# Optimization experiments

Measured on AMD Instinct MI355X. Metric: run time of the kernel, lower is better.

Reference implementation:

```python
import jax, jax.numpy as jnp
import numpy as np

NEG_BIG = 1e20


def setup_inputs() -> dict:
    key = jax.random.key(0)
    k1, k2, k3 = jax.random.split(key, 3)
    B, Tenc, Tdec, D = 8, 2048, 512, 1024
    enc = jax.random.normal(k1, (B, Tenc, D), dtype=jnp.float32)
    dec = jax.random.normal(k2, (B, Tdec, D), dtype=jnp.float32)
    enc_mask = jax.random.randint(k3, (B, Tenc), 0, 2, dtype=jnp.int32)
    # guarantee at least one valid position per row to keep softmax well-defined
    enc_mask = enc_mask.at[:, 0].set(1)
    return {"enc": enc, "enc_mask": enc_mask, "dec": dec}


def reference(enc, enc_mask, dec):
    # dropout=0 and identity transforms -> enc_trans = enc, dec_trans = dec
    mask = enc_mask.astype(enc.dtype)  # (B, Tenc)
    # raw scores: sum_d dec[b,u,d] * enc[b,t,d] -> (B, Tenc, Tdec)
    raw = jnp.einsum('btd,bud->btu', enc, dec)
    raw = raw - (1.0 - mask)[:, :, None] * NEG_BIG
    scores = jax.nn.softmax(raw, axis=1)  # softmax over Tenc
    # context: sum_t scores[b,t,u] * enc[b,t,d] -> (B, Tdec, D)
    context = jnp.einsum('btu,btd->bud', scores, enc)
    return context, scores
```

## Files before the change

kernel.cpp:

```cpp
#include <hip/hip_runtime.h>
#include <math.h>

#define BATCH 8
#define TENC 2048
#define TDEC 512
#define DIM 1024
#define NEG_BIG 1e20f

typedef __attribute__((ext_vector_type(8))) short short8;
typedef __attribute__((ext_vector_type(4))) float f32x4;
typedef unsigned short ushort_t;

__device__ __forceinline__ unsigned int bf16rn(float x) {
    unsigned int u = __float_as_uint(x);
    return (u + 0x7FFFu + ((u >> 16) & 1u)) >> 16;
}
__device__ __forceinline__ float bf16f(unsigned int b) {
    return __uint_as_float(b << 16);
}
__device__ __forceinline__ void split2(float x, unsigned int& h, unsigned int& l) {
    h = bf16rn(x);
    l = bf16rn(x - bf16f(h));
}

#define GLOAD16(g, l)                                                        \
    __builtin_amdgcn_global_load_lds(                                        \
        (const __attribute__((address_space(1))) unsigned int*)(g),          \
        (__attribute__((address_space(3))) unsigned int*)(l), 16, 0, 0)

__device__ __forceinline__ size_t tiled_off(int row, int k, int ntK) {
    return ((size_t)(row >> 4) * ntK + (k >> 5)) * 512
         + ((k >> 3) & 3) * 128 + (row & 15) * 8;
}


__global__ __launch_bounds__(256) void prep_fused(
    const float* __restrict__ enc, const float* __restrict__ dec,
    ushort_t* __restrict__ encH, ushort_t* __restrict__ encL,
    ushort_t* __restrict__ encT, ushort_t* __restrict__ decH,
    ushort_t* __restrict__ decL)
{
    __shared__ ushort_t T[64][72];

    const int b   = blockIdx.z;
    const int d0  = blockIdx.x * 64;
    const int tid = threadIdx.x;

    if (blockIdx.y < 32) {
        const int t0 = blockIdx.y * 64;
        const float* E = enc + (size_t)b * TENC * DIM;
        const size_t bofs1 = (size_t)b * TENC * DIM;
        const size_t bofs2 = (size_t)b * DIM * TENC;

        const int ltr = tid >> 2;
#pragma unroll
        for (int it = 0; it < 2; ++it) {
            const int c  = (tid & 3) + it * 4;
            const int gt = t0 + ltr;
            const int gd = d0 + c * 8;
            float4 x0 = *(const float4*)&E[(size_t)gt * DIM + gd];
            float4 x1 = *(const float4*)&E[(size_t)gt * DIM + gd + 4];
            float xs[8] = {x0.x, x0.y, x0.z, x0.w, x1.x, x1.y, x1.z, x1.w};
            unsigned int h[8], l[8];
            short8 hv, lv;
#pragma unroll
            for (int j = 0; j < 8; ++j) {
                split2(xs[j], h[j], l[j]);
                hv[j] = (short)h[j];
                lv[j] = (short)l[j];
            }
            const size_t off = bofs1 + tiled_off(gt, gd, DIM / 32);
            *(short8*)&encH[off] = hv;
            *(short8*)&encL[off] = lv;
#pragma unroll
            for (int j = 0; j < 8; ++j) T[c * 8 + j][ltr] = (ushort_t)h[j];
        }
        __syncthreads();

        const int dr = tid >> 2;
#pragma unroll
        for (int it = 0; it < 2; ++it) {
            const int tc = (tid & 3) + it * 4;
            const int gd = d0 + dr;
            const int gt = t0 + tc * 8;
            short8 v = *(const short8*)&T[dr][tc * 8];
            *(short8*)&encT[bofs2 + tiled_off(gd, gt, TENC / 32)] = v;
        }
    } else {
        const int u0 = (blockIdx.y - 32) * 64;
        const float* D = dec + (size_t)b * TDEC * DIM;
        const size_t bofs = (size_t)b * TDEC * DIM;

        const int lur = tid >> 2;
#pragma unroll
        for (int it = 0; it < 2; ++it) {
            const int c  = (tid & 3) + it * 4;
            const int gu = u0 + lur;
            const int gd = d0 + c * 8;
            float4 x0 = *(const float4*)&D[(size_t)gu * DIM + gd];
            float4 x1 = *(const float4*)&D[(size_t)gu * DIM + gd + 4];
            float xs[8] = {x0.x, x0.y, x0.z, x0.w, x1.x, x1.y, x1.z, x1.w};
            short8 hv, lv;
#pragma unroll
            for (int j = 0; j < 8; ++j) {
                unsigned int h, l;
                split2(xs[j], h, l);
                hv[j] = (short)h;
                lv[j] = (short)l;
            }
            const size_t off = bofs + tiled_off(gu, gd, DIM / 32);
            *(short8*)&decH[off] = hv;
            *(short8*)&decL[off] = lv;
        }
    }
}

__global__ __launch_bounds__(256) void gemm1_lds(
    const ushort_t* __restrict__ encH, const ushort_t* __restrict__ encL,
    const ushort_t* __restrict__ decH, const ushort_t* __restrict__ decL,
    const int* __restrict__ mask, float* __restrict__ raw,
    float* __restrict__ pm, float* __restrict__ ps)
{
    __shared__ __align__(16) ushort_t Ah[128 * 32];
    __shared__ __align__(16) ushort_t Al[128 * 32];
    __shared__ __align__(16) ushort_t Bh[128 * 32];
    __shared__ __align__(16) ushort_t Bl[128 * 32];
    __shared__ float smx[4][68];
    __shared__ float ssx[4][68];

    const int b  = blockIdx.x;
    const int m0 = blockIdx.y * 128;
    const int n0 = blockIdx.z * 128;
    const int tid = threadIdx.x;

    const int lane = tid & 63;
    const int w    = tid >> 6;
    const int wm   = (w & 1) * 64;
    const int wn   = (w >> 1) * 64;
    const int lr   = lane & 15;
    const int q    = lane >> 4;
    const int l8   = lane * 8;

    const int fa = wm * 32 + q * 128 + lr * 8;
    const int fb = wn * 32 + q * 128 + lr * 8;

    const ushort_t* AH = encH + (size_t)b * TENC * DIM;
    const ushort_t* AL = encL + (size_t)b * TENC * DIM;
    const ushort_t* BH = decH + (size_t)b * TDEC * DIM;
    const ushort_t* BL = decL + (size_t)b * TDEC * DIM;
    float* C = raw + (size_t)b * TENC * TDEC;

    f32x4 acc[4][4] = {};

    for (int k0 = 0; k0 < DIM; k0 += 32) {
        __syncthreads();
#pragma unroll
        for (int q2 = 0; q2 < 2; ++q2) {
            const int rg = w * 2 + q2;
            const size_t tA = ((size_t)((m0 >> 4) + rg) * (DIM / 32) + (k0 >> 5)) * 512 + l8;
            const size_t tB = ((size_t)((n0 >> 4) + rg) * (DIM / 32) + (k0 >> 5)) * 512 + l8;
            GLOAD16(AH + tA, &Ah[rg * 512]);
            GLOAD16(AL + tA, &Al[rg * 512]);
            GLOAD16(BH + tB, &Bh[rg * 512]);
            GLOAD16(BL + tB, &Bl[rg * 512]);
        }
        __syncthreads();

        short8 ah[4], al[4], bh[4], bl[4];
#pragma unroll
        for (int i = 0; i < 4; ++i) {
            ah[i] = *(const short8*)&Ah[fa + i * 512];
            al[i] = *(const short8*)&Al[fa + i * 512];
            bh[i] = *(const short8*)&Bh[fb + i * 512];
            bl[i] = *(const short8*)&Bl[fb + i * 512];
        }
#pragma unroll
        for (int i = 0; i < 4; ++i)
#pragma unroll
            for (int j = 0; j < 4; ++j) {
                acc[i][j] = __builtin_amdgcn_mfma_f32_16x16x32_bf16(ah[i], bh[j], acc[i][j], 0, 0, 0);
                acc[i][j] = __builtin_amdgcn_mfma_f32_16x16x32_bf16(ah[i], bl[j], acc[i][j], 0, 0, 0);
                acc[i][j] = __builtin_amdgcn_mfma_f32_16x16x32_bf16(al[i], bh[j], acc[i][j], 0, 0, 0);
            }
    }

    float mkv[4][4];
#pragma unroll
    for (int i = 0; i < 4; ++i)
#pragma unroll
        for (int rr = 0; rr < 4; ++rr) {
            const int t = m0 + wm + i * 16 + q * 4 + rr;
            mkv[i][rr] = (mask[b * TENC + t] == 0) ? NEG_BIG : 0.0f;
        }

    float cm[4] = {-INFINITY, -INFINITY, -INFINITY, -INFINITY};
    float cs[4] = {0.f, 0.f, 0.f, 0.f};
#pragma unroll
    for (int i = 0; i < 4; ++i)
#pragma unroll
        for (int rr = 0; rr < 4; ++rr) {
            const int t = m0 + wm + i * 16 + q * 4 + rr;
#pragma unroll
            for (int j = 0; j < 4; ++j) {
                const int u = n0 + wn + j * 16 + lr;
                const float v = acc[i][j][rr] - mkv[i][rr];
                C[(size_t)t * TDEC + u] = v;
                cm[j] = fmaxf(cm[j], v);
            }
        }
#pragma unroll
    for (int i = 0; i < 4; ++i)
#pragma unroll
        for (int rr = 0; rr < 4; ++rr)
#pragma unroll
            for (int j = 0; j < 4; ++j)
                cs[j] += __expf(acc[i][j][rr] - mkv[i][rr] - cm[j]);

#pragma unroll
    for (int j = 0; j < 4; ++j) {
#pragma unroll
        for (int d = 16; d < 64; d <<= 1) {
            float om = __shfl_xor(cm[j], d, 64);
            float os = __shfl_xor(cs[j], d, 64);
            float mn = fmaxf(cm[j], om);
            cs[j] = cs[j] * __expf(cm[j] - mn) + os * __expf(om - mn);
            cm[j] = mn;
        }
    }

    if (q == 0) {
#pragma unroll
        for (int j = 0; j < 4; ++j) {
            smx[w][j * 16 + lr] = cm[j];
            ssx[w][j * 16 + lr] = cs[j];
        }
    }
    __syncthreads();
    if (tid < 128) {
        const int col = tid;
        const int wp  = (col >> 6) * 2;
        const int ci  = col & 63;
        const float m1 = smx[wp][ci],     s1 = ssx[wp][ci];
        const float m2 = smx[wp + 1][ci], s2 = ssx[wp + 1][ci];
        const float M = fmaxf(m1, m2);
        const float S = s1 * __expf(m1 - M) + s2 * __expf(m2 - M);
        const int idx = b * TDEC + n0 + col;
        const int tb  = m0 >> 7;
        pm[(size_t)tb * (BATCH * TDEC) + idx] = M;
        ps[(size_t)tb * (BATCH * TDEC) + idx] = S;
    }
}

__global__ __launch_bounds__(256) void norm_kernel(
    float* __restrict__ S, const float* __restrict__ pm,
    const float* __restrict__ ps, ushort_t* __restrict__ scoresT)
{
    __shared__ ushort_t T[64][72];
    __shared__ float cMs[64], cIs[64];

    const int b  = blockIdx.z;
    const int t0 = blockIdx.x * 64;
    const int u0 = blockIdx.y * 64;
    const int tid = threadIdx.x;

    if (tid < 64) {
        const int idx = b * TDEC + u0 + tid;
        float M = -INFINITY;
#pragma unroll
        for (int z = 0; z < 16; ++z)
            M = fmaxf(M, pm[(size_t)z * (BATCH * TDEC) + idx]);
        float s = 0.0f;
#pragma unroll
        for (int z = 0; z < 16; ++z)
            s += ps[(size_t)z * (BATCH * TDEC) + idx] *
                 __expf(pm[(size_t)z * (BATCH * TDEC) + idx] - M);
        cMs[tid] = M;
        cIs[tid] = 1.0f / s;
    }
    __syncthreads();

    const int tr  = tid >> 4;
    const int ucl = (tid & 15) * 4;

    float4 M4 = *(const float4*)&cMs[ucl];
    float4 I4 = *(const float4*)&cIs[ucl];

    float* base = S + (size_t)b * TENC * TDEC;

#pragma unroll
    for (int i = 0; i < 4; ++i) {
        const int t = t0 + tr + 16 * i;
        float4 x = *(const float4*)&base[(size_t)t * TDEC + u0 + ucl];
        float4 p;
        p.x = __expf(x.x - M4.x) * I4.x;
        p.y = __expf(x.y - M4.y) * I4.y;
        p.z = __expf(x.z - M4.z) * I4.z;
        p.w = __expf(x.w - M4.w) * I4.w;
        *(float4*)&base[(size_t)t * TDEC + u0 + ucl] = p;
        const int tloc = tr + 16 * i;
        T[ucl + 0][tloc] = (ushort_t)bf16rn(p.x);
        T[ucl + 1][tloc] = (ushort_t)bf16rn(p.y);
        T[ucl + 2][tloc] = (ushort_t)bf16rn(p.z);
        T[ucl + 3][tloc] = (ushort_t)bf16rn(p.w);
    }
    __syncthreads();

    const size_t bofs = (size_t)b * TDEC * TENC;
    const int ur = tid >> 2;
#pragma unroll
    for (int it = 0; it < 2; ++it) {
        const int tc = (tid & 3) + it * 4;
        const int gu = u0 + ur;
        const int gt = t0 + tc * 8;
        short8 v = *(const short8*)&T[ur][tc * 8];
        *(short8*)&scoresT[bofs + tiled_off(gu, gt, TENC / 32)] = v;
    }
}

__global__ __launch_bounds__(256) void gemm2_lds(
    const ushort_t* __restrict__ scoresT, const ushort_t* __restrict__ encT,
    ushort_t* __restrict__ p0, ushort_t* __restrict__ p1,
    ushort_t* __restrict__ p2, ushort_t* __restrict__ p3)
{
    __shared__ __align__(16) ushort_t Ah[128 * 32];
    __shared__ __align__(16) ushort_t Bh[128 * 32];

    const int b  = blockIdx.x;
    const int ks = blockIdx.y >> 3;
    const int n0 = (blockIdx.y & 7) * 128;
    const int m0 = blockIdx.z * 128;
    const int tid = threadIdx.x;

    const int lane = tid & 63;
    const int w    = tid >> 6;
    const int wm   = (w & 1) * 64;
    const int wn   = (w >> 1) * 64;
    const int lr   = lane & 15;
    const int q    = lane >> 4;
    const int l8   = lane * 8;

    const int fa = wm * 32 + q * 128 + lr * 8;
    const int fb = wn * 32 + q * 128 + lr * 8;

    const ushort_t* A = scoresT + (size_t)b * TDEC * TENC;
    const ushort_t* B = encT    + (size_t)b * DIM * TENC;
    ushort_t* Psel = ks == 0 ? p0 : (ks == 1 ? p1 : (ks == 2 ? p2 : p3));
    ushort_t* P = Psel + (size_t)b * TDEC * DIM;

    const int kbeg = ks * (TENC / 4);
    const int kend = kbeg + TENC / 4;

    f32x4 acc[4][4] = {};

    for (int k0 = kbeg; k0 < kend; k0 += 32) {
        __syncthreads();
#pragma unroll
        for (int q2 = 0; q2 < 2; ++q2) {
            const int rg = w * 2 + q2;
            const size_t tA = ((size_t)((m0 >> 4) + rg) * (TENC / 32) + (k0 >> 5)) * 512 + l8;
            const size_t tB = ((size_t)((n0 >> 4) + rg) * (TENC / 32) + (k0 >> 5)) * 512 + l8;
            GLOAD16(A + tA, &Ah[rg * 512]);
            GLOAD16(B + tB, &Bh[rg * 512]);
        }
        __syncthreads();

        short8 ah[4], bh[4];
#pragma unroll
        for (int i = 0; i < 4; ++i) {
            ah[i] = *(const short8*)&Ah[fa + i * 512];
            bh[i] = *(const short8*)&Bh[fb + i * 512];
        }
#pragma unroll
        for (int i = 0; i < 4; ++i)
#pragma unroll
            for (int j = 0; j < 4; ++j)
                acc[i][j] = __builtin_amdgcn_mfma_f32_16x16x32_bf16(ah[i], bh[j], acc[i][j], 0, 0, 0);
    }

#pragma unroll
    for (int i = 0; i < 4; ++i)
#pragma unroll
        for (int rr = 0; rr < 4; ++rr) {
            const int u = m0 + wm + i * 16 + q * 4 + rr;
#pragma unroll
            for (int j = 0; j < 4; ++j) {
                const int d = n0 + wn + j * 16 + lr;
                P[(size_t)u * DIM + d] = (ushort_t)bf16rn(acc[i][j][rr]);
            }
        }
}

__global__ __launch_bounds__(256) void reduce_ctx(
    const ushort_t* __restrict__ p0, const ushort_t* __restrict__ p1,
    const ushort_t* __restrict__ p2, const ushort_t* __restrict__ p3,
    float* __restrict__ ctx)
{
    const size_t i8 = ((size_t)blockIdx.x * 256 + threadIdx.x) * 8;
    short8 a = *(const short8*)(p0 + i8);
    short8 b = *(const short8*)(p1 + i8);
    short8 c = *(const short8*)(p2 + i8);
    short8 d = *(const short8*)(p3 + i8);
    float o[8];
#pragma unroll
    for (int j = 0; j < 8; ++j)
        o[j] = bf16f((unsigned short)a[j]) + bf16f((unsigned short)b[j])
             + bf16f((unsigned short)c[j]) + bf16f((unsigned short)d[j]);
    *(float4*)(ctx + i8)     = make_float4(o[0], o[1], o[2], o[3]);
    *(float4*)(ctx + i8 + 4) = make_float4(o[4], o[5], o[6], o[7]);
}


__device__ __forceinline__ void store8(ushort_t* ph, ushort_t* pl,
                                       float4 x0, float4 x1) {
    float xs[8] = {x0.x, x0.y, x0.z, x0.w, x1.x, x1.y, x1.z, x1.w};
    short8 hv, lv;
#pragma unroll
    for (int i = 0; i < 8; ++i) {
        unsigned int h, l;
        split2(xs[i], h, l);
        hv[i] = (short)h;
        lv[i] = (short)l;
    }
    *(short8*)ph = hv;
    *(short8*)pl = lv;
}

__device__ __forceinline__ void wr4(ushort_t* ph, ushort_t* pl, const float* x) {
    unsigned int h[4], l[4];
#pragma unroll
    for (int i = 0; i < 4; ++i) split2(x[i], h[i], l[i]);
    *(uint2*)ph = make_uint2(h[0] | (h[1] << 16), h[2] | (h[3] << 16));
    *(uint2*)pl = make_uint2(l[0] | (l[1] << 16), l[2] | (l[3] << 16));
}

__device__ __forceinline__ short8 frag8B(const ushort_t* p) {
    union { short8 v; uint2 u[2]; } f;
    f.u[0] = *(const uint2*)p;
    f.u[1] = *(const uint2*)(p + 4);
    return f.v;
}

__global__ __launch_bounds__(256) void gemm1_mfma(
    const float* __restrict__ enc, const float* __restrict__ dec,
    const int* __restrict__ mask, float* __restrict__ raw)
{
    __shared__ __align__(16) ushort_t Ah[128 * 32];
    __shared__ __align__(16) ushort_t Al[128 * 32];
    __shared__ __align__(16) ushort_t Bh[128 * 32];
    __shared__ __align__(16) ushort_t Bl[128 * 32];

    const int b  = blockIdx.z;
    const int m0 = blockIdx.y * 128;
    const int n0 = blockIdx.x * 128;
    const int tid = threadIdx.x;

    const float* A  = enc + (size_t)b * TENC * DIM;
    const float* Bg = dec + (size_t)b * TDEC * DIM;
    float*       C  = raw + (size_t)b * TENC * TDEC;

    const int lane = tid & 63;
    const int wv   = tid >> 6;
    const int wm   = (wv & 1) * 64;
    const int wn   = (wv >> 1) * 64;
    const int lr   = lane & 15;
    const int q    = lane >> 4;

    const int r0 = tid >> 2;
    const int c8 = (tid & 3) * 8;

    f32x4 acc[4][4] = {};

    for (int k0 = 0; k0 < DIM; k0 += 32) {
        const float* pa0 = A  + (size_t)(m0 + r0) * DIM + k0 + c8;
        const float* pa1 = A  + (size_t)(m0 + r0 + 64) * DIM + k0 + c8;
        const float* pb0 = Bg + (size_t)(n0 + r0) * DIM + k0 + c8;
        const float* pb1 = Bg + (size_t)(n0 + r0 + 64) * DIM + k0 + c8;
        float4 a0 = *(const float4*)pa0, a0b = *(const float4*)(pa0 + 4);
        float4 a1 = *(const float4*)pa1, a1b = *(const float4*)(pa1 + 4);
        float4 b0 = *(const float4*)pb0, b0b = *(const float4*)(pb0 + 4);
        float4 b1 = *(const float4*)pb1, b1b = *(const float4*)(pb1 + 4);

        __syncthreads();
        store8(&Ah[r0 * 32 + c8],        &Al[r0 * 32 + c8],        a0, a0b);
        store8(&Ah[(r0 + 64) * 32 + c8], &Al[(r0 + 64) * 32 + c8], a1, a1b);
        store8(&Bh[r0 * 32 + c8],        &Bl[r0 * 32 + c8],        b0, b0b);
        store8(&Bh[(r0 + 64) * 32 + c8], &Bl[(r0 + 64) * 32 + c8], b1, b1b);
        __syncthreads();

        short8 ah[4], al[4], bh[4], bl[4];
#pragma unroll
        for (int i = 0; i < 4; ++i) {
            ah[i] = *(const short8*)&Ah[(wm + i * 16 + lr) * 32 + q * 8];
            al[i] = *(const short8*)&Al[(wm + i * 16 + lr) * 32 + q * 8];
            bh[i] = *(const short8*)&Bh[(wn + i * 16 + lr) * 32 + q * 8];
            bl[i] = *(const short8*)&Bl[(wn + i * 16 + lr) * 32 + q * 8];
        }
#pragma unroll
        for (int i = 0; i < 4; ++i)
#pragma unroll
            for (int j = 0; j < 4; ++j) {
                acc[i][j] = __builtin_amdgcn_mfma_f32_16x16x32_bf16(ah[i], bh[j], acc[i][j], 0, 0, 0);
                acc[i][j] = __builtin_amdgcn_mfma_f32_16x16x32_bf16(ah[i], bl[j], acc[i][j], 0, 0, 0);
                acc[i][j] = __builtin_amdgcn_mfma_f32_16x16x32_bf16(al[i], bh[j], acc[i][j], 0, 0, 0);
            }
    }

#pragma unroll
    for (int i = 0; i < 4; ++i)
#pragma unroll
        for (int rr = 0; rr < 4; ++rr) {
            const int t = m0 + wm + i * 16 + q * 4 + rr;
            const float mk = (mask[b * TENC + t] == 0) ? NEG_BIG : 0.0f;
#pragma unroll
            for (int j = 0; j < 4; ++j) {
                const int u = n0 + wn + j * 16 + lr;
                C[(size_t)t * TDEC + u] = acc[i][j][rr] - mk;
            }
        }
}

__global__ __launch_bounds__(256) void softmax_kernel(float* __restrict__ S)
{
    const int b  = blockIdx.y;
    const int u0 = blockIdx.x * 16;
    const int up = threadIdx.x & 15;
    const int tg = threadIdx.x >> 4;

    float* col = S + (size_t)b * TENC * TDEC + u0;

    float m = -INFINITY, s = 0.0f;
    for (int t = tg; t < TENC; t += 16) {
        float x = col[(size_t)t * TDEC + up];
        float mn = fmaxf(m, x);
        s = s * __expf(m - mn) + __expf(x - mn);
        m = mn;
    }

    __shared__ float sm[16][17];
    __shared__ float ss[16][17];
    sm[tg][up] = m;
    ss[tg][up] = s;
    __syncthreads();

    float M = -INFINITY;
#pragma unroll
    for (int j = 0; j < 16; ++j) M = fmaxf(M, sm[j][up]);
    float sum = 0.0f;
#pragma unroll
    for (int j = 0; j < 16; ++j) sum += ss[j][up] * __expf(sm[j][up] - M);
    const float inv = 1.0f / sum;

    for (int t = tg; t < TENC; t += 16) {
        float x = col[(size_t)t * TDEC + up];
        col[(size_t)t * TDEC + up] = __expf(x - M) * inv;
    }
}

#define G2_LD 36

__global__ __launch_bounds__(256) void gemm2_mfma(
    const float* __restrict__ scores, const float* __restrict__ enc,
    float* __restrict__ context)
{
    __shared__ __align__(16) ushort_t Ah[128 * G2_LD];
    __shared__ __align__(16) ushort_t Al[128 * G2_LD];
    __shared__ __align__(16) ushort_t Bh[128 * G2_LD];
    __shared__ __align__(16) ushort_t Bl[128 * G2_LD];

    const int b  = blockIdx.z;
    const int m0 = blockIdx.y * 128;
    const int n0 = blockIdx.x * 128;
    const int tid = threadIdx.x;

    const float* S = scores + (size_t)b * TENC * TDEC;
    const float* E = enc    + (size_t)b * TENC * DIM;
    float*       C = context + (size_t)b * TDEC * DIM;

    const int lane = tid & 63;
    const int wv   = tid >> 6;
    const int wm   = (wv & 1) * 64;
    const int wn   = (wv >> 1) * 64;
    const int lr   = lane & 15;
    const int q    = lane >> 4;

    const int ul = tid & 127;
    const int th = (tid >> 7) * 16;

    f32x4 acc[4][4] = {};

    for (int k0 = 0; k0 < TENC; k0 += 32) {
        float av[16], bv[16];
#pragma unroll
        for (int i = 0; i < 4; ++i) {
            const int t = k0 + th + i * 4;
#pragma unroll
            for (int j = 0; j < 4; ++j) {
                av[i * 4 + j] = S[(size_t)(t + j) * TDEC + m0 + ul];
                bv[i * 4 + j] = E[(size_t)(t + j) * DIM + n0 + ul];
            }
        }
        __syncthreads();
#pragma unroll
        for (int i = 0; i < 4; ++i) {
            const int tt = th + i * 4;
            wr4(&Ah[ul * G2_LD + tt], &Al[ul * G2_LD + tt], &av[i * 4]);
            wr4(&Bh[ul * G2_LD + tt], &Bl[ul * G2_LD + tt], &bv[i * 4]);
        }
        __syncthreads();

        short8 ah[4], al[4], bh[4], bl[4];
#pragma unroll
        for (int i = 0; i < 4; ++i) {
            ah[i] = frag8B(&Ah[(wm + i * 16 + lr) * G2_LD + q * 8]);
            al[i] = frag8B(&Al[(wm + i * 16 + lr) * G2_LD + q * 8]);
            bh[i] = frag8B(&Bh[(wn + i * 16 + lr) * G2_LD + q * 8]);
            bl[i] = frag8B(&Bl[(wn + i * 16 + lr) * G2_LD + q * 8]);
        }
#pragma unroll
        for (int i = 0; i < 4; ++i)
#pragma unroll
            for (int j = 0; j < 4; ++j) {
                acc[i][j] = __builtin_amdgcn_mfma_f32_16x16x32_bf16(ah[i], bh[j], acc[i][j], 0, 0, 0);
                acc[i][j] = __builtin_amdgcn_mfma_f32_16x16x32_bf16(ah[i], bl[j], acc[i][j], 0, 0, 0);
                acc[i][j] = __builtin_amdgcn_mfma_f32_16x16x32_bf16(al[i], bh[j], acc[i][j], 0, 0, 0);
            }
    }

#pragma unroll
    for (int i = 0; i < 4; ++i)
#pragma unroll
        for (int rr = 0; rr < 4; ++rr) {
            const int u = m0 + wm + i * 16 + q * 4 + rr;
#pragma unroll
            for (int j = 0; j < 4; ++j) {
                const int d = n0 + wn + j * 16 + lr;
                C[(size_t)u * DIM + d] = acc[i][j][rr];
            }
        }
}

extern "C" void kernel_launch(void* const* d_in, const int* in_sizes, int n_in,
                              void* d_out, int out_size, void* d_ws, size_t ws_size,
                              hipStream_t stream)
{
    const float* enc      = (const float*)d_in[0];
    const int*   enc_mask = (const int*)  d_in[1];
    const float* dec      = (const float*)d_in[2];

    float* context = (float*)d_out;
    float* scores  = context + (size_t)BATCH * TDEC * DIM;

    const size_t OFF_ENC_H = 0;
    const size_t OFF_ENC_L = 33554432;
    const size_t OFF_DEC_H = 67108864;
    const size_t OFF_DEC_L = 75497472;
    const size_t OFF_ENC_T = 83886080;
    const size_t OFF_SCO_T = 117440512;
    const size_t WS_NEED   = 134217728;

    if (ws_size >= WS_NEED) {
        char* w = (char*)d_ws;
        ushort_t* encH    = (ushort_t*)(w + OFF_ENC_H);
        ushort_t* encL    = (ushort_t*)(w + OFF_ENC_L);
        ushort_t* decH    = (ushort_t*)(w + OFF_DEC_H);
        ushort_t* decL    = (ushort_t*)(w + OFF_DEC_L);
        ushort_t* encT    = (ushort_t*)(w + OFF_ENC_T);
        ushort_t* scoresT = (ushort_t*)(w + OFF_SCO_T);
        ushort_t* part0   = (ushort_t*)(w + OFF_ENC_H);
        ushort_t* part1   = (ushort_t*)(w + OFF_ENC_H + 8388608);
        ushort_t* part2   = (ushort_t*)(w + OFF_ENC_H + 16777216);
        ushort_t* part3   = (ushort_t*)(w + OFF_ENC_H + 25165824);
        float*    pm      = context;
        float*    ps      = context + 65536;

        prep_fused<<<dim3(DIM / 64, 40, BATCH), 256, 0, stream>>>(
            enc, dec, encH, encL, encT, decH, decL);

        gemm1_lds<<<dim3(BATCH, TENC / 128, TDEC / 128), 256, 0, stream>>>(
            encH, encL, decH, decL, enc_mask, scores, pm, ps);

        norm_kernel<<<dim3(TENC / 64, TDEC / 64, BATCH), 256, 0, stream>>>(
            scores, pm, ps, scoresT);

        gemm2_lds<<<dim3(BATCH, 32, TDEC / 128), 256, 0, stream>>>(
            scoresT, encT, part0, part1, part2, part3);

        reduce_ctx<<<2048, 256, 0, stream>>>(part0, part1, part2, part3, context);
    } else {
        gemm1_mfma<<<dim3(TDEC / 128, TENC / 128, BATCH), 256, 0, stream>>>(
            enc, dec, enc_mask, scores);
        softmax_kernel<<<dim3(TDEC / 16, BATCH), 256, 0, stream>>>(scores);
        gemm2_mfma<<<dim3(DIM / 128, TDEC / 128, BATCH), 256, 0, stream>>>(
            scores, enc, context);
    }
}
```

Measured before the change: 233.2 us.

## Switch to fp16 split operands, store exp'd fp16 probabilities, widen gemm2 tile

Replaces the three-pass bf16 hi/lo split with fp16, keeping only enc high and dec high+low, so gemm1 issues two MFMAs per tile instead of three and no longer loads encL. Gemm1 now computes the block max first, then writes exp(x-M) as fp16 probabilities instead of fp32 raw scores. The norm kernel then only rescales by a per-block weight, which halves that intermediate traffic and avoids recomputing exp. Gemm2 uses 256-wide N tiles with fewer blocks and fp16 MFMA. The risks are fp16 range and precision loss in the scores, since small exp values can underflow, and higher register pressure in gemm2.

```diff
diff --git a/kernel.cpp b/kernel.cpp
--- a/kernel.cpp
+++ b/kernel.cpp
@@ -11,6 +11,17 @@
 typedef __attribute__((ext_vector_type(4))) float f32x4;
 typedef unsigned short ushort_t;
 
+__device__ __forceinline__ ushort_t f16bits(float x) {
+    union { _Float16 h; ushort_t u; } cv;
+    cv.h = (_Float16)x;
+    return cv.u;
+}
+__device__ __forceinline__ float f16val(ushort_t u) {
+    union { _Float16 h; ushort_t u; } cv;
+    cv.u = u;
+    return (float)cv.h;
+}
+
 __device__ __forceinline__ unsigned int bf16rn(float x) {
     unsigned int u = __float_as_uint(x);
     return (u + 0x7FFFu + ((u >> 16) & 1u)) >> 16;
@@ -36,9 +47,8 @@
 
 __global__ __launch_bounds__(256) void prep_fused(
     const float* __restrict__ enc, const float* __restrict__ dec,
-    ushort_t* __restrict__ encH, ushort_t* __restrict__ encL,
-    ushort_t* __restrict__ encT, ushort_t* __restrict__ decH,
-    ushort_t* __restrict__ decL)
+    ushort_t* __restrict__ encH, ushort_t* __restrict__ encT,
+    ushort_t* __restrict__ decH, ushort_t* __restrict__ decL)
 {
     __shared__ ushort_t T[64][72];
 
@@ -61,19 +71,12 @@
             float4 x0 = *(const float4*)&E[(size_t)gt * DIM + gd];
             float4 x1 = *(const float4*)&E[(size_t)gt * DIM + gd + 4];
             float xs[8] = {x0.x, x0.y, x0.z, x0.w, x1.x, x1.y, x1.z, x1.w};
-            unsigned int h[8], l[8];
-            short8 hv, lv;
-#pragma unroll
-            for (int j = 0; j < 8; ++j) {
-                split2(xs[j], h[j], l[j]);
-                hv[j] = (short)h[j];
-                lv[j] = (short)l[j];
-            }
-            const size_t off = bofs1 + tiled_off(gt, gd, DIM / 32);
-            *(short8*)&encH[off] = hv;
-            *(short8*)&encL[off] = lv;
-#pragma unroll
-            for (int j = 0; j < 8; ++j) T[c * 8 + j][ltr] = (ushort_t)h[j];
+            short8 hv;
+#pragma unroll
+            for (int j = 0; j < 8; ++j) hv[j] = (short)f16bits(xs[j]);
+            *(short8*)&encH[bofs1 + tiled_off(gt, gd, DIM / 32)] = hv;
+#pragma unroll
+            for (int j = 0; j < 8; ++j) T[c * 8 + j][ltr] = (ushort_t)hv[j];
         }
         __syncthreads();
 
@@ -81,10 +84,8 @@
 #pragma unroll
         for (int it = 0; it < 2; ++it) {
             const int tc = (tid & 3) + it * 4;
-            const int gd = d0 + dr;
-            const int gt = t0 + tc * 8;
             short8 v = *(const short8*)&T[dr][tc * 8];
-            *(short8*)&encT[bofs2 + tiled_off(gd, gt, TENC / 32)] = v;
+            *(short8*)&encT[bofs2 + tiled_off(d0 + dr, t0 + tc * 8, TENC / 32)] = v;
         }
     } else {
         const int u0 = (blockIdx.y - 32) * 64;
@@ -103,10 +104,9 @@
             short8 hv, lv;
 #pragma unroll
             for (int j = 0; j < 8; ++j) {
-                unsigned int h, l;
-                split2(xs[j], h, l);
+                ushort_t h = f16bits(xs[j]);
                 hv[j] = (short)h;
-                lv[j] = (short)l;
+                lv[j] = (short)f16bits(xs[j] - f16val(h));
             }
             const size_t off = bofs + tiled_off(gu, gd, DIM / 32);
             *(short8*)&decH[off] = hv;
@@ -116,13 +116,11 @@
 }
 
 __global__ __launch_bounds__(256) void gemm1_lds(
-    const ushort_t* __restrict__ encH, const ushort_t* __restrict__ encL,
-    const ushort_t* __restrict__ decH, const ushort_t* __restrict__ decL,
-    const int* __restrict__ mask, float* __restrict__ raw,
-    float* __restrict__ pm, float* __restrict__ ps)
+    const ushort_t* __restrict__ encH, const ushort_t* __restrict__ decH,
+    const ushort_t* __restrict__ decL, const int* __restrict__ mask,
+    ushort_t* __restrict__ p16, float* __restrict__ pm, float* __restrict__ ps)
 {
     __shared__ __align__(16) ushort_t Ah[128 * 32];
-    __shared__ __align__(16) ushort_t Al[128 * 32];
     __shared__ __align__(16) ushort_t Bh[128 * 32];
     __shared__ __align__(16) ushort_t Bl[128 * 32];
     __shared__ float smx[4][68];
@@ -145,10 +143,9 @@
     const int fb = wn * 32 + q * 128 + lr * 8;
 
     const ushort_t* AH = encH + (size_t)b * TENC * DIM;
-    const ushort_t* AL = encL + (size_t)b * TENC * DIM;
     const ushort_t* BH = decH + (size_t)b * TDEC * DIM;
     const ushort_t* BL = decL + (size_t)b * TDEC * DIM;
-    float* C = raw + (size_t)b * TENC * TDEC;
+    ushort_t* P = p16 + (size_t)b * TENC * TDEC;
 
     f32x4 acc[4][4] = {};
 
@@ -160,17 +157,15 @@
             const size_t tA = ((size_t)((m0 >> 4) + rg) * (DIM / 32) + (k0 >> 5)) * 512 + l8;
             const size_t tB = ((size_t)((n0 >> 4) + rg) * (DIM / 32) + (k0 >> 5)) * 512 + l8;
             GLOAD16(AH + tA, &Ah[rg * 512]);
-            GLOAD16(AL + tA, &Al[rg * 512]);
             GLOAD16(BH + tB, &Bh[rg * 512]);
             GLOAD16(BL + tB, &Bl[rg * 512]);
         }
         __syncthreads();
 
-        short8 ah[4], al[4], bh[4], bl[4];
+        short8 ah[4], bh[4], bl[4];
 #pragma unroll
         for (int i = 0; i < 4; ++i) {
             ah[i] = *(const short8*)&Ah[fa + i * 512];
-            al[i] = *(const short8*)&Al[fa + i * 512];
             bh[i] = *(const short8*)&Bh[fb + i * 512];
             bl[i] = *(const short8*)&Bl[fb + i * 512];
         }
@@ -178,9 +173,8 @@
         for (int i = 0; i < 4; ++i)
 #pragma unroll
             for (int j = 0; j < 4; ++j) {
-                acc[i][j] = __builtin_amdgcn_mfma_f32_16x16x32_bf16(ah[i], bh[j], acc[i][j], 0, 0, 0);
-                acc[i][j] = __builtin_amdgcn_mfma_f32_16x16x32_bf16(ah[i], bl[j], acc[i][j], 0, 0, 0);
-                acc[i][j] = __builtin_amdgcn_mfma_f32_16x16x32_bf16(al[i], bh[j], acc[i][j], 0, 0, 0);
+                acc[i][j] = __builtin_amdgcn_mfma_f32_16x16x32_f16(ah[i], bh[j], acc[i][j], 0, 0, 0);
+                acc[i][j] = __builtin_amdgcn_mfma_f32_16x16x32_f16(ah[i], bl[j], acc[i][j], 0, 0, 0);
             }
     }
 
@@ -194,6 +188,28 @@
         }
 
     float cm[4] = {-INFINITY, -INFINITY, -INFINITY, -INFINITY};
+#pragma unroll
+    for (int i = 0; i < 4; ++i)
+#pragma unroll
+        for (int rr = 0; rr < 4; ++rr)
+#pragma unroll
+            for (int j = 0; j < 4; ++j)
+                cm[j] = fmaxf(cm[j], acc[i][j][rr] - mkv[i][rr]);
+#pragma unroll
+    for (int j = 0; j < 4; ++j) {
+        cm[j] = fmaxf(cm[j], __shfl_xor(cm[j], 16, 64));
+        cm[j] = fmaxf(cm[j], __shfl_xor(cm[j], 32, 64));
+    }
+    if (q == 0) {
+#pragma unroll
+        for (int j = 0; j < 4; ++j) smx[w][j * 16 + lr] = cm[j];
+    }
+    __syncthreads();
+    float M[4];
+#pragma unroll
+    for (int j = 0; j < 4; ++j)
+        M[j] = fmaxf(smx[w][j * 16 + lr], smx[w ^ 1][j * 16 + lr]);
+
     float cs[4] = {0.f, 0.f, 0.f, 0.f};
 #pragma unroll
     for (int i = 0; i < 4; ++i)
@@ -203,64 +219,46 @@
 #pragma unroll
             for (int j = 0; j < 4; ++j) {
                 const int u = n0 + wn + j * 16 + lr;
-                const float v = acc[i][j][rr] - mkv[i][rr];
-                C[(size_t)t * TDEC + u] = v;
-                cm[j] = fmaxf(cm[j], v);
-            }
-        }
-#pragma unroll
-    for (int i = 0; i < 4; ++i)
-#pragma unroll
-        for (int rr = 0; rr < 4; ++rr)
-#pragma unroll
-            for (int j = 0; j < 4; ++j)
-                cs[j] += __expf(acc[i][j][rr] - mkv[i][rr] - cm[j]);
-
+                const float p = __expf(acc[i][j][rr] - mkv[i][rr] - M[j]);
+                cs[j] += p;
+                P[(size_t)t * TDEC + u] = f16bits(p);
+            }
+        }
 #pragma unroll
     for (int j = 0; j < 4; ++j) {
-#pragma unroll
-        for (int d = 16; d < 64; d <<= 1) {
-            float om = __shfl_xor(cm[j], d, 64);
-            float os = __shfl_xor(cs[j], d, 64);
-            float mn = fmaxf(cm[j], om);
-            cs[j] = cs[j] * __expf(cm[j] - mn) + os * __expf(om - mn);
-            cm[j] = mn;
-        }
-    }
-
+        cs[j] += __shfl_xor(cs[j], 16, 64);
+        cs[j] += __shfl_xor(cs[j], 32, 64);
+    }
     if (q == 0) {
 #pragma unroll
-        for (int j = 0; j < 4; ++j) {
-            smx[w][j * 16 + lr] = cm[j];
-            ssx[w][j * 16 + lr] = cs[j];
-        }
+        for (int j = 0; j < 4; ++j) ssx[w][j * 16 + lr] = cs[j];
     }
     __syncthreads();
     if (tid < 128) {
         const int col = tid;
         const int wp  = (col >> 6) * 2;
         const int ci  = col & 63;
-        const float m1 = smx[wp][ci],     s1 = ssx[wp][ci];
-        const float m2 = smx[wp + 1][ci], s2 = ssx[wp + 1][ci];
-        const float M = fmaxf(m1, m2);
-        const float S = s1 * __expf(m1 - M) + s2 * __expf(m2 - M);
+        const float Mf = fmaxf(smx[wp][ci], smx[wp + 1][ci]);
+        const float Sf = ssx[wp][ci] + ssx[wp + 1][ci];
         const int idx = b * TDEC + n0 + col;
         const int tb  = m0 >> 7;
-        pm[(size_t)tb * (BATCH * TDEC) + idx] = M;
-        ps[(size_t)tb * (BATCH * TDEC) + idx] = S;
+        pm[(size_t)tb * (BATCH * TDEC) + idx] = Mf;
+        ps[(size_t)tb * (BATCH * TDEC) + idx] = Sf;
     }
 }
 
 __global__ __launch_bounds__(256) void norm_kernel(
-    float* __restrict__ S, const float* __restrict__ pm,
-    const float* __restrict__ ps, ushort_t* __restrict__ scoresT)
+    const ushort_t* __restrict__ p16, float* __restrict__ scores,
+    const float* __restrict__ pm, const float* __restrict__ ps,
+    ushort_t* __restrict__ scoresT)
 {
     __shared__ ushort_t T[64][72];
-    __shared__ float cMs[64], cIs[64];
+    __shared__ float cW[64];
 
     const int b  = blockIdx.z;
     const int t0 = blockIdx.x * 64;
     const int u0 = blockIdx.y * 64;
+    const int tb = t0 >> 7;
     const int tid = threadIdx.x;
 
     if (tid < 64) {
@@ -274,34 +272,34 @@
         for (int z = 0; z < 16; ++z)
             s += ps[(size_t)z * (BATCH * TDEC) + idx] *
                  __expf(pm[(size_t)z * (BATCH * TDEC) + idx] - M);
-        cMs[tid] = M;
-        cIs[tid] = 1.0f / s;
+        cW[tid] = __expf(pm[(size_t)tb * (BATCH * TDEC) + idx] - M) / s;
     }
     __syncthreads();
 
     const int tr  = tid >> 4;
     const int ucl = (tid & 15) * 4;
 
-    float4 M4 = *(const float4*)&cMs[ucl];
-    float4 I4 = *(const float4*)&cIs[ucl];
-
-    float* base = S + (size_t)b * TENC * TDEC;
+    const float w0 = cW[ucl + 0], w1 = cW[ucl + 1];
+    const float w2 = cW[ucl + 2], w3 = cW[ucl + 3];
+
+    const ushort_t* Pb = p16 + (size_t)b * TENC * TDEC;
+    float* Sb = scores + (size_t)b * TENC * TDEC;
 
 #pragma unroll
     for (int i = 0; i < 4; ++i) {
         const int t = t0 + tr + 16 * i;
-        float4 x = *(const float4*)&base[(size_t)t * TDEC + u0 + ucl];
-        float4 p;
-        p.x = __expf(x.x - M4.x) * I4.x;
-        p.y = __expf(x.y - M4.y) * I4.y;
-        p.z = __expf(x.z - M4.z) * I4.z;
-        p.w = __expf(x.w - M4.w) * I4.w;
-        *(float4*)&base[(size_t)t * TDEC + u0 + ucl] = p;
+        ushort4 pv = *(const ushort4*)&Pb[(size_t)t * TDEC + u0 + ucl];
+        float4 sc;
+        sc.x = f16val(pv.x) * w0;
+        sc.y = f16val(pv.y) * w1;
+        sc.z = f16val(pv.z) * w2;
+        sc.w = f16val(pv.w) * w3;
+        *(float4*)&Sb[(size_t)t * TDEC + u0 + ucl] = sc;
         const int tloc = tr + 16 * i;
-        T[ucl + 0][tloc] = (ushort_t)bf16rn(p.x);
-        T[ucl + 1][tloc] = (ushort_t)bf16rn(p.y);
-        T[ucl + 2][tloc] = (ushort_t)bf16rn(p.z);
-        T[ucl + 3][tloc] = (ushort_t)bf16rn(p.w);
+        T[ucl + 0][tloc] = f16bits(sc.x);
+        T[ucl + 1][tloc] = f16bits(sc.y);
+        T[ucl + 2][tloc] = f16bits(sc.z);
+        T[ucl + 3][tloc] = f16bits(sc.w);
     }
     __syncthreads();
 
@@ -310,10 +308,8 @@
 #pragma unroll
     for (int it = 0; it < 2; ++it) {
         const int tc = (tid & 3) + it * 4;
-        const int gu = u0 + ur;
-        const int gt = t0 + tc * 8;
         short8 v = *(const short8*)&T[ur][tc * 8];
-        *(short8*)&scoresT[bofs + tiled_off(gu, gt, TENC / 32)] = v;
+        *(short8*)&scoresT[bofs + tiled_off(u0 + ur, t0 + tc * 8, TENC / 32)] = v;
     }
 }
 
@@ -323,18 +319,18 @@
     ushort_t* __restrict__ p2, ushort_t* __restrict__ p3)
 {
     __shared__ __align__(16) ushort_t Ah[128 * 32];
-    __shared__ __align__(16) ushort_t Bh[128 * 32];
+    __shared__ __align__(16) ushort_t Bh[256 * 32];
 
     const int b  = blockIdx.x;
-    const int ks = blockIdx.y >> 3;
-    const int n0 = (blockIdx.y & 7) * 128;
+    const int ks = blockIdx.y >> 2;
+    const int n0 = (blockIdx.y & 3) * 256;
     const int m0 = blockIdx.z * 128;
     const int tid = threadIdx.x;
 
     const int lane = tid & 63;
     const int w    = tid >> 6;
     const int wm   = (w & 1) * 64;
-    const int wn   = (w >> 1) * 64;
+    const int wn   = (w >> 1) * 128;
     const int lr   = lane & 15;
     const int q    = lane >> 4;
     const int l8   = lane * 8;
@@ -350,7 +346,7 @@
     const int kbeg = ks * (TENC / 4);
     const int kend = kbeg + TENC / 4;
 
-    f32x4 acc[4][4] = {};
+    f32x4 acc[4][8] = {};
 
     for (int k0 = kbeg; k0 < kend; k0 += 32) {
         __syncthreads();
@@ -358,23 +354,26 @@
         for (int q2 = 0; q2 < 2; ++q2) {
             const int rg = w * 2 + q2;
             const size_t tA = ((size_t)((m0 >> 4) + rg) * (TENC / 32) + (k0 >> 5)) * 512 + l8;
+            GLOAD16(A + tA, &Ah[rg * 512]);
+        }
+#pragma unroll
+        for (int q2 = 0; q2 < 4; ++q2) {
+            const int rg = w * 4 + q2;
             const size_t tB = ((size_t)((n0 >> 4) + rg) * (TENC / 32) + (k0 >> 5)) * 512 + l8;
-            GLOAD16(A + tA, &Ah[rg * 512]);
             GLOAD16(B + tB, &Bh[rg * 512]);
         }
         __syncthreads();
 
-        short8 ah[4], bh[4];
-#pragma unroll
-        for (int i = 0; i < 4; ++i) {
-            ah[i] = *(const short8*)&Ah[fa + i * 512];
-            bh[i] = *(const short8*)&Bh[fb + i * 512];
-        }
+        short8 av[4], bv[8];
+#pragma unroll
+        for (int i = 0; i < 4; ++i) av[i] = *(const short8*)&Ah[fa + i * 512];
+#pragma unroll
+        for (int j = 0; j < 8; ++j) bv[j] = *(const short8*)&Bh[fb + j * 512];
 #pragma unroll
         for (int i = 0; i < 4; ++i)
 #pragma unroll
-            for (int j = 0; j < 4; ++j)
-                acc[i][j] = __builtin_amdgcn_mfma_f32_16x16x32_bf16(ah[i], bh[j], acc[i][j], 0, 0, 0);
+            for (int j = 0; j < 8; ++j)
+                acc[i][j] = __builtin_amdgcn_mfma_f32_16x16x32_f16(av[i], bv[j], acc[i][j], 0, 0, 0);
     }
 
 #pragma unroll
@@ -383,9 +382,9 @@
         for (int rr = 0; rr < 4; ++rr) {
             const int u = m0 + wm + i * 16 + q * 4 + rr;
 #pragma unroll
-            for (int j = 0; j < 4; ++j) {
+            for (int j = 0; j < 8; ++j) {
                 const int d = n0 + wn + j * 16 + lr;
-                P[(size_t)u * DIM + d] = (ushort_t)bf16rn(acc[i][j][rr]);
+                P[(size_t)u * DIM + d] = f16bits(acc[i][j][rr]);
             }
         }
 }
@@ -403,8 +402,8 @@
     float o[8];
 #pragma unroll
     for (int j = 0; j < 8; ++j)
-        o[j] = bf16f((unsigned short)a[j]) + bf16f((unsigned short)b[j])
-             + bf16f((unsigned short)c[j]) + bf16f((unsigned short)d[j]);
+        o[j] = f16val((ushort_t)a[j]) + f16val((ushort_t)b[j])
+             + f16val((ushort_t)c[j]) + f16val((ushort_t)d[j]);
     *(float4*)(ctx + i8)     = make_float4(o[0], o[1], o[2], o[3]);
     *(float4*)(ctx + i8 + 4) = make_float4(o[4], o[5], o[6], o[7]);
 }
@@ -651,7 +650,7 @@
     float* scores  = context + (size_t)BATCH * TDEC * DIM;
 
     const size_t OFF_ENC_H = 0;
-    const size_t OFF_ENC_L = 33554432;
+    const size_t OFF_P16   = 33554432;
     const size_t OFF_DEC_H = 67108864;
     const size_t OFF_DEC_L = 75497472;
     const size_t OFF_ENC_T = 83886080;
@@ -661,7 +660,7 @@
     if (ws_size >= WS_NEED) {
         char* w = (char*)d_ws;
         ushort_t* encH    = (ushort_t*)(w + OFF_ENC_H);
-        ushort_t* encL    = (ushort_t*)(w + OFF_ENC_L);
+        ushort_t* p16     = (ushort_t*)(w + OFF_P16);
         ushort_t* decH    = (ushort_t*)(w + OFF_DEC_H);
         ushort_t* decL    = (ushort_t*)(w + OFF_DEC_L);
         ushort_t* encT    = (ushort_t*)(w + OFF_ENC_T);
@@ -674,15 +673,15 @@
         float*    ps      = context + 65536;
 
         prep_fused<<<dim3(DIM / 64, 40, BATCH), 256, 0, stream>>>(
-            enc, dec, encH, encL, encT, decH, decL);
+            enc, dec, encH, encT, decH, decL);
 
         gemm1_lds<<<dim3(BATCH, TENC / 128, TDEC / 128), 256, 0, stream>>>(
-            encH, encL, decH, decL, enc_mask, scores, pm, ps);
+            encH, decH, decL, enc_mask, p16, pm, ps);
 
         norm_kernel<<<dim3(TENC / 64, TDEC / 64, BATCH), 256, 0, stream>>>(
-            scores, pm, ps, scoresT);
-
-        gemm2_lds<<<dim3(BATCH, 32, TDEC / 128), 256, 0, stream>>>(
+            p16, scores, pm, ps, scoresT);
+
+        gemm2_lds<<<dim3(BATCH, 16, TDEC / 128), 256, 0, stream>>>(
             scoresT, encT, part0, part1, part2, part3);
 
         reduce_ctx<<<2048, 256, 0, stream>>>(part0, part1, part2, part3, context);
```

After: 227.2 us. 1.03x faster.
